# Kernel tuning notes

Measured on AMD Instinct MI355X. Metric: run time of the kernel, lower is better.

Reference implementation:

```python
import jax, jax.numpy as jnp
import numpy as np

COMMITMENT = 0.25

def setup_inputs() -> dict:
    key = jax.random.key(0)
    k1, k2 = jax.random.split(key)
    x = jax.random.normal(k1, (64, 256, 32, 32), dtype=jnp.float32)
    embed = jax.random.normal(k2, (256, 1024), dtype=jnp.float32)  # [emb_dim, num_emb]
    return {"x": x, "embed": embed}

def reference(x, embed):
    # x: [B, C, H, W] -> NHWC
    xt = jnp.transpose(x, (0, 2, 3, 1))              # [B, H, W, C]
    B, H, W, C = xt.shape
    flat = xt.reshape(-1, C)                         # [N, C]
    # squared euclidean distances to each codebook column
    dist = (jnp.sum(flat * flat, axis=1, keepdims=True)
            - 2.0 * flat @ embed
            + jnp.sum(embed * embed, axis=0, keepdims=True))  # [N, num_emb]
    embed_idx = jnp.argmin(dist, axis=1).reshape(B, H, W)     # [B, H, W]
    quantize = embed.T[embed_idx]                    # [B, H, W, C]
    e_latent_loss = jnp.mean((jax.lax.stop_gradient(quantize) - xt) ** 2)
    q_latent_loss = jnp.mean((quantize - jax.lax.stop_gradient(xt)) ** 2)
    loss = q_latent_loss + COMMITMENT * e_latent_loss
    # straight-through estimator
    quantize = xt + jax.lax.stop_gradient(quantize - xt)
    quantize = jnp.transpose(quantize, (0, 3, 1, 2))  # back to NCHW
    return quantize, loss, embed_idx
```

## Files before the change

kernel.cpp:

```cpp
#include <hip/hip_runtime.h>

#define CDIM 256
#define HW   1024
#define NPIX 65536
#define KDIM 1024
#define TAU  0.5f
#define RB   4
#define SWZ(c) (((c) & 31) ^ (((c) >> 3) & 24))

using bf16x8 = __attribute__((ext_vector_type(8))) short;
using f32x4  = __attribute__((ext_vector_type(4))) float;
typedef unsigned int u32;

static __device__ __forceinline__ unsigned short f2bf(float v) {
    union { float f; unsigned u; } a; a.f = v;
    unsigned u = a.u;
    u += 0x7fffu + ((u >> 16) & 1u);
    return (unsigned short)(u >> 16);
}

static __device__ __forceinline__ void gload_lds16(const void* g, void* s) {
    __builtin_amdgcn_global_load_lds(
        (const __attribute__((address_space(1))) u32*)g,
        (__attribute__((address_space(3))) u32*)s,
        16, 0, 0);
}

__global__ void ee_kernel(const float* __restrict__ embed, float* __restrict__ ee) {
    int k = blockIdx.x * 256 + threadIdx.x;
    float s = 0.f;
#pragma unroll 8
    for (int c = 0; c < CDIM; ++c) {
        float v = embed[c * KDIM + k];
        s += v * v;
    }
    ee[k] = s;
}

__global__ void transpose_e(const float* __restrict__ embed, float* __restrict__ embedT) {
    __shared__ float tl[32][33];
    const int t = threadIdx.x;
    const int j = t & 31, r = t >> 5;
    const int k0 = (blockIdx.x & 31) * 32;
    const int c0 = (blockIdx.x >> 5) * 32;
#pragma unroll
    for (int rr = 0; rr < 4; ++rr) {
        int c = r * 4 + rr;
        tl[c][j] = embed[(size_t)(c0 + c) * KDIM + k0 + j];
    }
    __syncthreads();
#pragma unroll
    for (int rr = 0; rr < 4; ++rr) {
        int k = r * 4 + rr;
        embedT[(size_t)(k0 + k) * CDIM + c0 + j] = tl[j][k];
    }
}

__global__ void prep_e(const float* __restrict__ embed, short* __restrict__ e_hi) {
    int tid = blockIdx.x * 256 + threadIdx.x;
    int l  = tid & 63;
    int f  = tid >> 6;
    int nf = f & 3;
    int ks = (f >> 2) & 7;
    int nh = (f >> 5) & 1;
    int nt = f >> 6;
    int n  = nt * 128 + (nh * 4 + nf) * 16 + (l & 15);
    int c0 = ks * 32 + (l >> 4) * 8;
    bf16x8 h8;
#pragma unroll
    for (int j = 0; j < 8; ++j)
        h8[j] = (short)f2bf(-2.0f * embed[(c0 + j) * KDIM + n]);
    *(bf16x8*)&e_hi[(size_t)tid * 8] = h8;
}

__launch_bounds__(256, 2)
__global__ void vq_gemm(const float* __restrict__ x, const short* __restrict__ e_hi,
                        const float* __restrict__ ee,
                        float* __restrict__ hv1, float* __restrict__ hv2,
                        int* __restrict__ hidx) {
    __shared__ short Bs[2][8192];
    const int t  = threadIdx.x;
    const int l  = t & 63;
    const int w  = t >> 6;
    const int lr = l & 15;
    const int lg = l >> 4;
    const int tile = blockIdx.x & 255;
    const int half = blockIdx.x >> 8;
    const int px0 = tile * 256 + w * 64;
    const int b   = px0 >> 10;
    const int p0  = px0 & 1023;
    const float* xb = x + (size_t)b * CDIM * HW;

    const int c_first = half * 16;
    {
        const int slab = w * 4;
        const char* srcb = (const char*)e_hi +
            (size_t)(((c_first >> 2) * 2 + ((c_first >> 1) & 1)) * 32 + (c_first & 1) * 2) * 1024 + l * 16;
        char* dstb = (char*)&Bs[0][0] + (size_t)slab * 1024 + l * 16;
#pragma unroll
        for (int i = 0; i < 4; ++i) {
            int s = slab + i;
            gload_lds16(srcb + (size_t)((s >> 1) * 4 + (s & 1)) * 1024, dstb + (size_t)i * 1024);
        }
    }

    bf16x8 a[4][8];
#pragma unroll
    for (int mf = 0; mf < 4; ++mf) {
#pragma unroll
        for (int ks = 0; ks < 8; ++ks) {
            const float* p = xb + (size_t)(ks * 32 + lg * 8) * HW + p0 + mf * 16 + lr;
            float v[8];
#pragma unroll
            for (int j = 0; j < 8; ++j) v[j] = p[(size_t)j * HW];
#pragma unroll
            for (int j = 0; j < 8; ++j) a[mf][ks][j] = (short)f2bf(v[j]);
        }
    }

    float minv[16], min2v[16];
    int   mini[16];
#pragma unroll
    for (int r = 0; r < 16; ++r) { minv[r] = 3.4e38f; min2v[r] = 3.4e38f; mini[r] = 0; }

    __syncthreads();

    for (int cc = 0; cc < 16; ++cc) {
        const int c   = c_first + cc;
        const int cur = cc & 1;
        if (cc < 15) {
            const int cn = c + 1;
            const int slab = w * 4;
            const char* srcb = (const char*)e_hi +
                (size_t)(((cn >> 2) * 2 + ((cn >> 1) & 1)) * 32 + (cn & 1) * 2) * 1024 + l * 16;
            char* dstb = (char*)&Bs[cur ^ 1][0] + (size_t)slab * 1024 + l * 16;
#pragma unroll
            for (int i = 0; i < 4; ++i) {
                int s = slab + i;
                gload_lds16(srcb + (size_t)((s >> 1) * 4 + (s & 1)) * 1024, dstb + (size_t)i * 1024);
            }
        }

        f32x4 acc[4][2];
#pragma unroll
        for (int mf = 0; mf < 4; ++mf)
#pragma unroll
            for (int nfi = 0; nfi < 2; ++nfi)
                acc[mf][nfi] = (f32x4){0.f, 0.f, 0.f, 0.f};

#pragma unroll
        for (int ks = 0; ks < 8; ++ks) {
#pragma unroll
            for (int nfi = 0; nfi < 2; ++nfi) {
                bf16x8 bh = *(const bf16x8*)&Bs[cur][((ks * 2 + nfi) * 64 + l) * 8];
#pragma unroll
                for (int mf = 0; mf < 4; ++mf)
                    acc[mf][nfi] = __builtin_amdgcn_mfma_f32_16x16x32_bf16(a[mf][ks], bh, acc[mf][nfi], 0, 0, 0);
            }
        }

#pragma unroll
        for (int nfi = 0; nfi < 2; ++nfi) {
            const int kg = c * 32 + nfi * 16 + lr;
            const float eev = ee[kg];
#pragma unroll
            for (int mf = 0; mf < 4; ++mf)
#pragma unroll
                for (int j = 0; j < 4; ++j) {
                    const int r = mf * 4 + j;
                    float m = acc[mf][nfi][j] + eev;
                    bool lt = m < minv[r];
                    float sec = lt ? minv[r] : m;
                    minv[r] = lt ? m : minv[r];
                    mini[r] = lt ? kg : mini[r];
                    min2v[r] = fminf(min2v[r], sec);
                }
        }
        __syncthreads();
    }

#pragma unroll
    for (int r = 0; r < 16; ++r) {
        float v1 = minv[r]; int i1 = mini[r]; float v2 = min2v[r];
#pragma unroll
        for (int mask = 1; mask < 16; mask <<= 1) {
            float ov1 = __shfl_xor(v1, mask, 64);
            int   oi1 = __shfl_xor(i1, mask, 64);
            float ov2 = __shfl_xor(v2, mask, 64);
            float vmax = fmaxf(v1, ov1);
            v2 = fminf(fminf(v2, ov2), vmax);
            bool take = (ov1 < v1) || (ov1 == v1 && oi1 < i1);
            v1 = take ? ov1 : v1;
            i1 = take ? oi1 : i1;
        }
        if (lr == 0) {
            int px = px0 + (r >> 2) * 16 + lg * 4 + (r & 3);
            int o = half * NPIX + px;
            hv1[o] = v1; hv2[o] = v2; hidx[o] = i1;
        }
    }
}

__global__ void merge_halves(const float* __restrict__ hv1, const float* __restrict__ hv2,
                             const int* __restrict__ hidx, int* __restrict__ idx_out,
                             int* __restrict__ worklist, int* __restrict__ wcount) {
    int px = blockIdx.x * 256 + threadIdx.x;
    float va = hv1[px],        vb = hv1[NPIX + px];
    float sa = hv2[px],        sb = hv2[NPIX + px];
    int   ia = hidx[px],       ib = hidx[NPIX + px];
    bool aw = va <= vb;
    float v1 = aw ? va : vb;
    int   i1 = aw ? ia : ib;
    float v2 = fminf(aw ? sa : sb, aw ? vb : va);
    idx_out[px] = i1;
    if (v2 - v1 < TAU) {
        int pos = atomicAdd(wcount, 1);
        worklist[pos] = px;
    }
}

__launch_bounds__(256)
__global__ void vq_rescue(const float* __restrict__ x, const float* __restrict__ embed,
                          const float* __restrict__ ee,
                          const int* __restrict__ worklist, const int* __restrict__ wcount,
                          int* __restrict__ idx_out) {
    __shared__ float xs[RB][CDIM];
    __shared__ int   pxs[RB];
    __shared__ float redv[4][RB];
    __shared__ int   redi[4][RB];
    const int t  = threadIdx.x;
    const int wv = t >> 6, ln = t & 63;
    const int cnt = *wcount;
    for (int base = blockIdx.x * RB; base < cnt; base += gridDim.x * RB) {
        const int nb = min(RB, cnt - base);
        __syncthreads();
        if (t < RB) pxs[t] = worklist[base + (t < nb ? t : nb - 1)];
        __syncthreads();
#pragma unroll
        for (int i = 0; i < RB; ++i) {
            int gn = pxs[i];
            xs[i][t] = x[(size_t)(gn >> 10) * CDIM * HW + (size_t)t * HW + (gn & 1023)];
        }
        __syncthreads();

        float4 acc[RB];
#pragma unroll
        for (int i = 0; i < RB; ++i) acc[i] = make_float4(0.f, 0.f, 0.f, 0.f);
#pragma unroll 4
        for (int c = 0; c < CDIM; ++c) {
            float4 ev = *(const float4*)&embed[c * KDIM + t * 4];
#pragma unroll
            for (int i = 0; i < RB; ++i) {
                float xv = xs[i][c];
                acc[i].x = fmaf(xv, ev.x, acc[i].x);
                acc[i].y = fmaf(xv, ev.y, acc[i].y);
                acc[i].z = fmaf(xv, ev.z, acc[i].z);
                acc[i].w = fmaf(xv, ev.w, acc[i].w);
            }
        }
        const float4 eev = *(const float4*)&ee[t * 4];
#pragma unroll
        for (int i = 0; i < RB; ++i) {
            float d0 = fmaf(-2.f, acc[i].x, eev.x);
            float d1 = fmaf(-2.f, acc[i].y, eev.y);
            float d2 = fmaf(-2.f, acc[i].z, eev.z);
            float d3 = fmaf(-2.f, acc[i].w, eev.w);
            float v = d0; int ix = t * 4;
            if (d1 < v) { v = d1; ix = t * 4 + 1; }
            if (d2 < v) { v = d2; ix = t * 4 + 2; }
            if (d3 < v) { v = d3; ix = t * 4 + 3; }
#pragma unroll
            for (int mask = 1; mask < 64; mask <<= 1) {
                float ov = __shfl_xor(v, mask, 64);
                int   oi = __shfl_xor(ix, mask, 64);
                bool take = (ov < v) || (ov == v && oi < ix);
                v = take ? ov : v; ix = take ? oi : ix;
            }
            if (ln == 0) { redv[wv][i] = v; redi[wv][i] = ix; }
        }
        __syncthreads();
        if (t < nb) {
            float fv = redv[0][t]; int fi = redi[0][t];
#pragma unroll
            for (int q = 1; q < 4; ++q) {
                float v = redv[q][t]; int ix = redi[q][t];
                if (v < fv || (v == fv && ix < fi)) { fv = v; fi = ix; }
            }
            idx_out[pxs[t]] = fi;
        }
    }
}

__launch_bounds__(256)
__global__ void vq_epilogue(const float* __restrict__ x, const float* __restrict__ embed,
                            const float* __restrict__ embedT, int useT,
                            const int* __restrict__ idx_in, float* __restrict__ out_q,
                            float* __restrict__ out_idx, float* __restrict__ partials) {
    __shared__ float q[16384];
    __shared__ int   idxs[128];
    __shared__ float lred[4];
    const int t = threadIdx.x;
    const int w = t >> 6, l = t & 63;
    const int n0 = blockIdx.x * 128;
    const int b  = n0 >> 10;

    if (t < 128) idxs[t] = idx_in[n0 + t];
    __syncthreads();
    if (t < 128) out_idx[n0 + t] = (float)idxs[t];

    const int j  = t >> 2;
    const int qd = t & 3;
    float lsum = 0.f;

#pragma unroll
    for (int pass = 0; pass < 2; ++pass) {
        const int myidx = idxs[pass * 64 + j];
        if (useT) {
            const float4* src4 = (const float4*)embedT + (size_t)myidx * 64;
#pragma unroll
            for (int i = 0; i < 16; ++i) {
                float4 v = src4[qd * 16 + i];
                int c = qd * 64 + i * 4;
                q[(c + 0) * 64 + (j ^ SWZ(c + 0))] = v.x;
                q[(c + 1) * 64 + (j ^ SWZ(c + 1))] = v.y;
                q[(c + 2) * 64 + (j ^ SWZ(c + 2))] = v.z;
                q[(c + 3) * 64 + (j ^ SWZ(c + 3))] = v.w;
            }
        } else {
#pragma unroll 4
            for (int i = 0; i < 64; ++i) {
                int c = qd * 64 + i;
                q[c * 64 + (j ^ SWZ(c))] = embed[(size_t)c * KDIM + myidx];
            }
        }
        __syncthreads();

        const int p0 = (n0 & 1023) + pass * 64;
        const size_t xbase = (size_t)b * CDIM * HW + p0;
#pragma unroll 8
        for (int ci = 0; ci < 64; ++ci) {
            int c = w * 64 + ci;
            float qv = q[c * 64 + (l ^ SWZ(c))];
            float xv = x[xbase + (size_t)c * HW + l];
            out_q[xbase + (size_t)c * HW + l] = qv;
            float d = qv - xv;
            lsum = fmaf(d, d, lsum);
        }
        __syncthreads();
    }

#pragma unroll
    for (int off = 32; off > 0; off >>= 1)
        lsum += __shfl_down(lsum, off, 64);
    if (l == 0) lred[w] = lsum;
    __syncthreads();
    if (t == 0)
        partials[blockIdx.x] = (lred[0] + lred[1]) + (lred[2] + lred[3]);
}

__global__ void loss_kernel(const float* __restrict__ partials, float* __restrict__ out_loss) {
    __shared__ float s[256];
    s[threadIdx.x] = partials[threadIdx.x] + partials[threadIdx.x + 256];
    __syncthreads();
    for (int off = 128; off > 0; off >>= 1) {
        if (threadIdx.x < off) s[threadIdx.x] += s[threadIdx.x + off];
        __syncthreads();
    }
    if (threadIdx.x == 0)
        out_loss[0] = 1.25f * s[0] / 16777216.0f;
}

extern "C" void kernel_launch(void* const* d_in, const int* in_sizes, int n_in,
                              void* d_out, int out_size, void* d_ws, size_t ws_size,
                              hipStream_t stream) {
    const float* x     = (const float*)d_in[0];
    const float* embed = (const float*)d_in[1];
    float* out_q    = (float*)d_out;
    float* out_loss = out_q + (size_t)NPIX * CDIM;
    float* out_idx  = out_loss + 1;
    int*   idx_i32  = (int*)out_idx;

    short* e_hi     = (short*)out_q;
    int*   worklist = (int*)(out_q + 131072);
    float* hv1      = out_q + 196608;
    float* hv2      = out_q + 327680;
    int*   hidx     = (int*)(out_q + 458752);

    float* ws       = (float*)d_ws;
    float* ee       = ws;
    int*   wcount   = (int*)(ws + 1024);
    float* partials = ws + 1088;
    float* embedT   = ws + 1600;
    int useT = (ws_size >= (size_t)(1600 + 262144) * sizeof(float)) ? 1 : 0;

    ee_kernel<<<KDIM / 256, 256, 0, stream>>>(embed, ee);
    if (useT) transpose_e<<<256, 256, 0, stream>>>(embed, embedT);
    prep_e<<<128, 256, 0, stream>>>(embed, e_hi);
    hipMemsetAsync(wcount, 0, 4, stream);
    vq_gemm<<<512, 256, 0, stream>>>(x, e_hi, ee, hv1, hv2, hidx);
    merge_halves<<<NPIX / 256, 256, 0, stream>>>(hv1, hv2, hidx, idx_i32, worklist, wcount);
    vq_rescue<<<1024, 256, 0, stream>>>(x, embed, ee, worklist, wcount, idx_i32);
    vq_epilogue<<<NPIX / 128, 256, 0, stream>>>(x, embed, useT ? embedT : embed, useT,
                                                idx_i32, out_q, out_idx, partials);
    loss_kernel<<<1, 256, 0, stream>>>(partials, out_loss);
}
```

Baseline: 154.2 us.

## Compute loss from min distances plus ||x||^2 instead of rereading x in epilogue

The GEMM kernel now accumulates each pixel's squared norm while it loads x. The merge and rescue steps store the per-pixel min distance plus that norm, which equals ||q-x||^2. The loss is then reduced from this buffer by two small kernels, so the epilogue no longer reads x and only gathers and writes the codebook rows. This removes a full 64 MB read of x from the epilogue, but the loss now depends on the bf16-approximated GEMM distances for pixels that are not rescued, which can change accuracy. Rescue batch size and grid are also doubled.

```diff
diff --git a/kernel.cpp b/kernel.cpp
--- a/kernel.cpp
+++ b/kernel.cpp
@@ -5,7 +5,7 @@
 #define NPIX 65536
 #define KDIM 1024
 #define TAU  0.5f
-#define RB   4
+#define RB   8
 #define SWZ(c) (((c) & 31) ^ (((c) >> 3) & 24))
 
 using bf16x8 = __attribute__((ext_vector_type(8))) short;
@@ -77,7 +77,7 @@
 __global__ void vq_gemm(const float* __restrict__ x, const short* __restrict__ e_hi,
                         const float* __restrict__ ee,
                         float* __restrict__ hv1, float* __restrict__ hv2,
-                        int* __restrict__ hidx) {
+                        int* __restrict__ hidx, float* __restrict__ xxbuf) {
     __shared__ short Bs[2][8192];
     const int t  = threadIdx.x;
     const int l  = t & 63;
@@ -105,6 +105,7 @@
     }
 
     bf16x8 a[4][8];
+    float xxp[4] = {0.f, 0.f, 0.f, 0.f};
 #pragma unroll
     for (int mf = 0; mf < 4; ++mf) {
 #pragma unroll
@@ -114,8 +115,20 @@
 #pragma unroll
             for (int j = 0; j < 8; ++j) v[j] = p[(size_t)j * HW];
 #pragma unroll
+            for (int j = 0; j < 8; ++j) xxp[mf] = fmaf(v[j], v[j], xxp[mf]);
+#pragma unroll
             for (int j = 0; j < 8; ++j) a[mf][ks][j] = (short)f2bf(v[j]);
         }
+    }
+#pragma unroll
+    for (int mf = 0; mf < 4; ++mf) {
+        xxp[mf] += __shfl_xor(xxp[mf], 16, 64);
+        xxp[mf] += __shfl_xor(xxp[mf], 32, 64);
+    }
+    if (half == 0 && l < 16) {
+#pragma unroll
+        for (int mf = 0; mf < 4; ++mf)
+            xxbuf[px0 + mf * 16 + l] = xxp[mf];
     }
 
     float minv[16], min2v[16];
@@ -202,7 +215,8 @@
 }
 
 __global__ void merge_halves(const float* __restrict__ hv1, const float* __restrict__ hv2,
-                             const int* __restrict__ hidx, int* __restrict__ idx_out,
+                             const int* __restrict__ hidx, const float* __restrict__ xxbuf,
+                             int* __restrict__ idx_out, float* __restrict__ d_buf,
                              int* __restrict__ worklist, int* __restrict__ wcount) {
     int px = blockIdx.x * 256 + threadIdx.x;
     float va = hv1[px],        vb = hv1[NPIX + px];
@@ -213,6 +227,7 @@
     int   i1 = aw ? ia : ib;
     float v2 = fminf(aw ? sa : sb, aw ? vb : va);
     idx_out[px] = i1;
+    d_buf[px] = v1 + xxbuf[px];
     if (v2 - v1 < TAU) {
         int pos = atomicAdd(wcount, 1);
         worklist[pos] = px;
@@ -221,9 +236,9 @@
 
 __launch_bounds__(256)
 __global__ void vq_rescue(const float* __restrict__ x, const float* __restrict__ embed,
-                          const float* __restrict__ ee,
+                          const float* __restrict__ ee, const float* __restrict__ xxbuf,
                           const int* __restrict__ worklist, const int* __restrict__ wcount,
-                          int* __restrict__ idx_out) {
+                          int* __restrict__ idx_out, float* __restrict__ d_buf) {
     __shared__ float xs[RB][CDIM];
     __shared__ int   pxs[RB];
     __shared__ float redv[4][RB];
@@ -286,19 +301,44 @@
                 float v = redv[q][t]; int ix = redi[q][t];
                 if (v < fv || (v == fv && ix < fi)) { fv = v; fi = ix; }
             }
-            idx_out[pxs[t]] = fi;
-        }
-    }
+            int gn = pxs[t];
+            idx_out[gn] = fi;
+            d_buf[gn] = fv + xxbuf[gn];
+        }
+    }
+}
+
+__global__ void loss1_kernel(const float* __restrict__ d_buf, float* __restrict__ partials) {
+    __shared__ float s[4];
+    const int t = threadIdx.x;
+    float v = d_buf[blockIdx.x * 256 + t];
+#pragma unroll
+    for (int off = 32; off > 0; off >>= 1)
+        v += __shfl_down(v, off, 64);
+    if ((t & 63) == 0) s[t >> 6] = v;
+    __syncthreads();
+    if (t == 0) partials[blockIdx.x] = (s[0] + s[1]) + (s[2] + s[3]);
+}
+
+__global__ void loss2_kernel(const float* __restrict__ partials, float* __restrict__ out_loss) {
+    __shared__ float s[256];
+    s[threadIdx.x] = partials[threadIdx.x];
+    __syncthreads();
+    for (int off = 128; off > 0; off >>= 1) {
+        if (threadIdx.x < off) s[threadIdx.x] += s[threadIdx.x + off];
+        __syncthreads();
+    }
+    if (threadIdx.x == 0)
+        out_loss[0] = 1.25f * s[0] / 16777216.0f;
 }
 
 __launch_bounds__(256)
-__global__ void vq_epilogue(const float* __restrict__ x, const float* __restrict__ embed,
+__global__ void vq_epilogue(const float* __restrict__ embed,
                             const float* __restrict__ embedT, int useT,
                             const int* __restrict__ idx_in, float* __restrict__ out_q,
-                            float* __restrict__ out_idx, float* __restrict__ partials) {
+                            float* __restrict__ out_idx) {
     __shared__ float q[16384];
     __shared__ int   idxs[128];
-    __shared__ float lred[4];
     const int t = threadIdx.x;
     const int w = t >> 6, l = t & 63;
     const int n0 = blockIdx.x * 128;
@@ -310,7 +350,6 @@
 
     const int j  = t >> 2;
     const int qd = t & 3;
-    float lsum = 0.f;
 
 #pragma unroll
     for (int pass = 0; pass < 2; ++pass) {
@@ -340,34 +379,10 @@
 #pragma unroll 8
         for (int ci = 0; ci < 64; ++ci) {
             int c = w * 64 + ci;
-            float qv = q[c * 64 + (l ^ SWZ(c))];
-            float xv = x[xbase + (size_t)c * HW + l];
-            out_q[xbase + (size_t)c * HW + l] = qv;
-            float d = qv - xv;
-            lsum = fmaf(d, d, lsum);
-        }
-        __syncthreads();
-    }
-
-#pragma unroll
-    for (int off = 32; off > 0; off >>= 1)
-        lsum += __shfl_down(lsum, off, 64);
-    if (l == 0) lred[w] = lsum;
-    __syncthreads();
-    if (t == 0)
-        partials[blockIdx.x] = (lred[0] + lred[1]) + (lred[2] + lred[3]);
-}
-
-__global__ void loss_kernel(const float* __restrict__ partials, float* __restrict__ out_loss) {
-    __shared__ float s[256];
-    s[threadIdx.x] = partials[threadIdx.x] + partials[threadIdx.x + 256];
-    __syncthreads();
-    for (int off = 128; off > 0; off >>= 1) {
-        if (threadIdx.x < off) s[threadIdx.x] += s[threadIdx.x + off];
-        __syncthreads();
-    }
-    if (threadIdx.x == 0)
-        out_loss[0] = 1.25f * s[0] / 16777216.0f;
+            out_q[xbase + (size_t)c * HW + l] = q[c * 64 + (l ^ SWZ(c))];
+        }
+        __syncthreads();
+    }
 }
 
 extern "C" void kernel_launch(void* const* d_in, const int* in_sizes, int n_in,
@@ -385,6 +400,8 @@
     float* hv1      = out_q + 196608;
     float* hv2      = out_q + 327680;
     int*   hidx     = (int*)(out_q + 458752);
+    float* xxbuf    = out_q + 589824;
+    float* d_buf    = out_q + 655360;
 
     float* ws       = (float*)d_ws;
     float* ee       = ws;
@@ -397,10 +414,12 @@
     if (useT) transpose_e<<<256, 256, 0, stream>>>(embed, embedT);
     prep_e<<<128, 256, 0, stream>>>(embed, e_hi);
     hipMemsetAsync(wcount, 0, 4, stream);
-    vq_gemm<<<512, 256, 0, stream>>>(x, e_hi, ee, hv1, hv2, hidx);
-    merge_halves<<<NPIX / 256, 256, 0, stream>>>(hv1, hv2, hidx, idx_i32, worklist, wcount);
-    vq_rescue<<<1024, 256, 0, stream>>>(x, embed, ee, worklist, wcount, idx_i32);
-    vq_epilogue<<<NPIX / 128, 256, 0, stream>>>(x, embed, useT ? embedT : embed, useT,
-                                                idx_i32, out_q, out_idx, partials);
-    loss_kernel<<<1, 256, 0, stream>>>(partials, out_loss);
-}
+    vq_gemm<<<512, 256, 0, stream>>>(x, e_hi, ee, hv1, hv2, hidx, xxbuf);
+    merge_halves<<<NPIX / 256, 256, 0, stream>>>(hv1, hv2, hidx, xxbuf, idx_i32, d_buf,
+                                                 worklist, wcount);
+    vq_rescue<<<2048, 256, 0, stream>>>(x, embed, ee, xxbuf, worklist, wcount, idx_i32, d_buf);
+    loss1_kernel<<<NPIX / 256, 256, 0, stream>>>(d_buf, partials);
+    loss2_kernel<<<1, 256, 0, stream>>>(partials, out_loss);
+    vq_epilogue<<<NPIX / 128, 256, 0, stream>>>(embed, useT ? embedT : embed, useT,
+                                                idx_i32, out_q, out_idx);
+}
```

Result: slower. 184.0 us (+19.4%).
